# Kernel tuning notes

Measured on AMD Instinct MI355X. Metric: run time of the kernel, lower is better.

The kernel has to match this reference:

```python
import jax, jax.numpy as jnp
import numpy as np

D_MODEL = 1024
NUM_HEADS = 16
D_K = D_MODEL // NUM_HEADS
D_FF = 4096
EPS = 1e-5


def setup_inputs() -> dict:
    key = jax.random.key(0)
    ks = jax.random.split(key, 16)
    B, S = 2, 2048
    s_attn = 1.0 / np.sqrt(D_MODEL)
    s_ff1 = 1.0 / np.sqrt(D_MODEL)
    s_ff2 = 1.0 / np.sqrt(D_FF)
    return {
        "x": jax.random.normal(ks[0], (B, S, D_MODEL), jnp.float32),
        "Wq": jax.random.normal(ks[1], (D_MODEL, D_MODEL), jnp.float32) * s_attn,
        "bq": jnp.zeros((D_MODEL,), jnp.float32),
        "Wk": jax.random.normal(ks[2], (D_MODEL, D_MODEL), jnp.float32) * s_attn,
        "bk": jnp.zeros((D_MODEL,), jnp.float32),
        "Wv": jax.random.normal(ks[3], (D_MODEL, D_MODEL), jnp.float32) * s_attn,
        "bv": jnp.zeros((D_MODEL,), jnp.float32),
        "Wo": jax.random.normal(ks[4], (D_MODEL, D_MODEL), jnp.float32) * s_attn,
        "bo": jnp.zeros((D_MODEL,), jnp.float32),
        "W1": jax.random.normal(ks[5], (D_MODEL, D_FF), jnp.float32) * s_ff1,
        "b1": jnp.zeros((D_FF,), jnp.float32),
        "W2": jax.random.normal(ks[6], (D_FF, D_MODEL), jnp.float32) * s_ff2,
        "b2": jnp.zeros((D_MODEL,), jnp.float32),
        "g1": jnp.ones((D_MODEL,), jnp.float32),
        "be1": jnp.zeros((D_MODEL,), jnp.float32),
        "g2": jnp.ones((D_MODEL,), jnp.float32),
        "be2": jnp.zeros((D_MODEL,), jnp.float32),
    }


def _layernorm(x, g, b):
    m = jnp.mean(x, axis=-1, keepdims=True)
    v = jnp.mean(jnp.square(x - m), axis=-1, keepdims=True)
    return (x - m) * jax.lax.rsqrt(v + EPS) * g + b


def _split_heads(x, B, S):
    # (B, S, D) -> (B, H, S, d_k)
    return x.reshape(B, S, NUM_HEADS, D_K).transpose(0, 2, 1, 3)


def reference(x, Wq, bq, Wk, bk, Wv, bv, Wo, bo, W1, b1, W2, b2, g1, be1, g2, be2):
    B, S, _ = x.shape
    Q = _split_heads(x @ Wq + bq, B, S)
    K = _split_heads(x @ Wk + bk, B, S)
    V = _split_heads(x @ Wv + bv, B, S)
    scores = jnp.einsum("bhqd,bhkd->bhqk", Q, K) / np.sqrt(D_K).astype(np.float32)
    attn = jax.nn.softmax(scores, axis=-1)  # dropout is identity (p=0 / eval)
    ctx = jnp.einsum("bhqk,bhkd->bhqd", attn, V)
    ctx = ctx.transpose(0, 2, 1, 3).reshape(B, S, D_MODEL)
    attn_out = ctx @ Wo + bo
    h = _layernorm(x + attn_out, g1, be1)
    ff = jax.nn.relu(h @ W1 + b1) @ W2 + b2
    out = _layernorm(h + ff, g2, be2)
    return out, attn
```

## Files before the change

kernel.cpp:

```cpp
#include <hip/hip_runtime.h>
#include <cstddef>
#include <cstdint>

#define D_MODEL 1024
#define NUM_HEADS 16
#define DK 64
#define D_FF 4096
#define SEQ 2048
#define BATCH 2
#define EPS 1e-5f

typedef unsigned short u16;
typedef __attribute__((ext_vector_type(8))) short bf16x8;
typedef __attribute__((ext_vector_type(8))) unsigned short us8;
typedef __attribute__((ext_vector_type(4))) unsigned short us4;
typedef __attribute__((ext_vector_type(4))) float f32x4;

#define SBAR() asm volatile("s_barrier" ::: "memory")

__device__ __forceinline__ u16 f2b(float f) {
    unsigned u = __float_as_uint(f);
    u += 0x7fffu + ((u >> 16) & 1u);
    return (u16)(u >> 16);
}
__device__ __forceinline__ float b2f(u16 v) {
    return __uint_as_float((unsigned)v << 16);
}

__device__ __forceinline__ void gload16(const void* g, void* l) {
    __builtin_amdgcn_global_load_lds(
        (const __attribute__((address_space(1))) void*)g,
        (__attribute__((address_space(3))) void*)l, 16, 0, 0);
}

__device__ __forceinline__ void stage_half(
    const u16* __restrict__ g, int ld, long kbase, int h,
    u16* dst, int tid, int wid)
{
#pragma unroll
    for (int r = 0; r < 2; ++r) {
        const int ci  = r * 512 + tid;
        const int row = ci >> 2;
        const int wd  = ci & 3;
        const int f   = (row + (row >> 2)) & 3;
        const long src = (long)row * ld + kbase + (long)(h * 4 + (wd ^ f)) * 8;
        gload16(g + src, dst + (r * 512 + wid * 64) * 8);
    }
}

__device__ __forceinline__ bf16x8 frag64(const u16* base, int ks, int row, int g) {
    const int f = (row + (row >> 2)) & 3;
    return *(const bf16x8*)&base[ks * 8192 + row * 32 + ((g ^ f) * 8)];
}

template<int KTOT, bool RELU>
__global__ __launch_bounds__(512, 2) void gemm256(
    const u16* __restrict__ Abf, const u16* __restrict__ BT,
    const float* __restrict__ bias0, u16* __restrict__ C0,
    int ldc, int nx)
{
    constexpr int NT = KTOT / 64;
    __shared__ u16 lds[2][32768];

    const int tid = threadIdx.x;
    const int wid = tid >> 6, l = tid & 63;
    const int r16 = l & 15, g = l >> 4;
    const int wr = wid >> 2, wc = wid & 3;

    const int nwg = gridDim.x;
    const int q = nwg >> 3, rr = nwg & 7;
    const int xcd = blockIdx.x & 7, idx = blockIdx.x >> 3;
    const int wg = (xcd < rr ? xcd * (q + 1) : rr * (q + 1) + (xcd - rr) * q) + idx;
    const long bm = (long)(wg / nx) * 256;
    const long bn = (long)(wg % nx) * 256;

    const u16* Ag = Abf + bm * KTOT;
    const u16* Bg = BT + bn * KTOT;

    f32x4 acc[8][4];
#pragma unroll
    for (int i = 0; i < 8; ++i)
#pragma unroll
        for (int n = 0; n < 4; ++n)
            acc[i][n] = (f32x4){0.f, 0.f, 0.f, 0.f};

    stage_half(Ag, KTOT, 0, 0, &lds[0][0],     tid, wid);
    stage_half(Ag, KTOT, 0, 1, &lds[0][8192],  tid, wid);
    stage_half(Bg, KTOT, 0, 0, &lds[0][16384], tid, wid);
    stage_half(Bg, KTOT, 0, 1, &lds[0][24576], tid, wid);
    if (NT > 1) {
        stage_half(Ag, KTOT, 64, 0, &lds[1][0],     tid, wid);
        stage_half(Bg, KTOT, 64, 0, &lds[1][16384], tid, wid);
    }
    asm volatile("s_waitcnt vmcnt(4)" ::: "memory");
    SBAR();

    for (int t = 0; t < NT; ++t) {
        u16* cur = &lds[t & 1][0];
        u16* nxt = &lds[(t + 1) & 1][0];
        const long k1 = (long)(t + 1) * 64;
        const long k2 = (long)(t + 2) * 64;
        const bool s1 = (t + 1 < NT), s2 = (t + 2 < NT);

        bf16x8 a0[4], b0[4];
#pragma unroll
        for (int i = 0; i < 4; ++i) {
            a0[i] = frag64(cur,         0, wr * 128 + i * 16 + r16, g);
            b0[i] = frag64(cur + 16384, 0, wc * 64  + i * 16 + r16, g);
        }
        if (s1) stage_half(Ag, KTOT, k1, 1, nxt + 8192, tid, wid);
        SBAR();
        __builtin_amdgcn_s_setprio(1);
#pragma unroll
        for (int i = 0; i < 4; ++i)
#pragma unroll
            for (int n = 0; n < 4; ++n)
                acc[i][n] = __builtin_amdgcn_mfma_f32_16x16x32_bf16(
                    a0[i], b0[n], acc[i][n], 0, 0, 0);
        __builtin_amdgcn_s_setprio(0);
        SBAR();

        bf16x8 a1[4];
#pragma unroll
        for (int i = 0; i < 4; ++i)
            a1[i] = frag64(cur, 0, wr * 128 + (i + 4) * 16 + r16, g);
        if (s1) stage_half(Bg, KTOT, k1, 1, nxt + 24576, tid, wid);
        SBAR();
        __builtin_amdgcn_s_setprio(1);
#pragma unroll
        for (int i = 0; i < 4; ++i)
#pragma unroll
            for (int n = 0; n < 4; ++n)
                acc[i + 4][n] = __builtin_amdgcn_mfma_f32_16x16x32_bf16(
                    a1[i], b0[n], acc[i + 4][n], 0, 0, 0);
        __builtin_amdgcn_s_setprio(0);
        SBAR();

        bf16x8 a2[4], b1[4];
#pragma unroll
        for (int i = 0; i < 4; ++i) {
            a2[i] = frag64(cur,         1, wr * 128 + i * 16 + r16, g);
            b1[i] = frag64(cur + 16384, 1, wc * 64  + i * 16 + r16, g);
        }
        if (s2) stage_half(Ag, KTOT, k2, 0, cur, tid, wid);
        SBAR();
        __builtin_amdgcn_s_setprio(1);
#pragma unroll
        for (int i = 0; i < 4; ++i)
#pragma unroll
            for (int n = 0; n < 4; ++n)
                acc[i][n] = __builtin_amdgcn_mfma_f32_16x16x32_bf16(
                    a2[i], b1[n], acc[i][n], 0, 0, 0);
        __builtin_amdgcn_s_setprio(0);
        SBAR();

        bf16x8 a3[4];
#pragma unroll
        for (int i = 0; i < 4; ++i)
            a3[i] = frag64(cur, 1, wr * 128 + (i + 4) * 16 + r16, g);
        if (s2) stage_half(Bg, KTOT, k2, 0, cur + 16384, tid, wid);
        SBAR();
        __builtin_amdgcn_s_setprio(1);
#pragma unroll
        for (int i = 0; i < 4; ++i)
#pragma unroll
            for (int n = 0; n < 4; ++n)
                acc[i + 4][n] = __builtin_amdgcn_mfma_f32_16x16x32_bf16(
                    a3[i], b1[n], acc[i + 4][n], 0, 0, 0);
        __builtin_amdgcn_s_setprio(0);
        if (s2)      asm volatile("s_waitcnt vmcnt(4)" ::: "memory");
        else if (s1) asm volatile("s_waitcnt vmcnt(0)" ::: "memory");
        SBAR();
    }

    const long crow0 = bm + wr * 128 + g * 4;
    const long ccol0 = bn + wc * 64 + r16;
#pragma unroll
    for (int n = 0; n < 4; ++n) {
        const long col = ccol0 + n * 16;
        const float bv = bias0[col];
#pragma unroll
        for (int i = 0; i < 8; ++i)
#pragma unroll
            for (int j = 0; j < 4; ++j) {
                const long row = crow0 + i * 16 + j;
                float v = acc[i][n][j] + bv;
                if (RELU) v = fmaxf(v, 0.f);
                C0[row * (long)ldc + col] = f2b(v);
            }
    }
}

template<bool RELU, int NSPLIT>
__global__ __launch_bounds__(256) void gemm_mfma(
    const u16* __restrict__ Abf, const u16* __restrict__ BT,
    const float* __restrict__ bias0, const float* __restrict__ bias1,
    const float* __restrict__ bias2,
    u16* __restrict__ C0, u16* __restrict__ C1, u16* __restrict__ C2,
    int lda, int ldb, int ldc, int K, int nx)
{
    constexpr int BM = 128, BN = 128;
    constexpr int MI = 4, NI = 4;
    constexpr int RA = 2, RB = 2;
    constexpr int TILE = (BM + BN) * 32;

    __shared__ u16 sm[2][TILE];

    const int tid = threadIdx.x;
    const int w = tid >> 6, l = tid & 63;
    const int r16 = l & 15, g = l >> 4;
    const int wr = w >> 1, wc = w & 1;

    const int nwg = gridDim.x;
    const int q = nwg >> 3, rr = nwg & 7;
    const int xcd = blockIdx.x & 7, idx = blockIdx.x >> 3;
    const int wg = (xcd < rr ? xcd * (q + 1) : rr * (q + 1) + (xcd - rr) * q) + idx;
    const long bm = (long)(wg / nx) * BM;
    const long bn = (long)(wg % nx) * BN;

    f32x4 acc[MI][NI];
#pragma unroll
    for (int mi = 0; mi < MI; ++mi)
#pragma unroll
        for (int ni = 0; ni < NI; ++ni)
            acc[mi][ni] = (f32x4){0.f, 0.f, 0.f, 0.f};

    long aOff[RA], bOff[RB];
#pragma unroll
    for (int r = 0; r < RA; ++r) {
        int c = r * 256 + tid;
        aOff[r] = (long)(bm + (c >> 2)) * lda + (c & 3) * 8;
    }
#pragma unroll
    for (int r = 0; r < RB; ++r) {
        int c = r * 256 + tid;
        bOff[r] = (long)(bn + (c >> 2)) * ldb + (c & 3) * 8;
    }

#pragma unroll
    for (int r = 0; r < RA; ++r)
        gload16(Abf + aOff[r], &sm[0][0] + (r * 256 + w * 64) * 8);
#pragma unroll
    for (int r = 0; r < RB; ++r)
        gload16(BT + bOff[r], &sm[0][BM * 32] + (r * 256 + w * 64) * 8);
    __syncthreads();

    int cur = 0;
    for (int k0 = 0; k0 < K; k0 += 32) {
        if (k0 + 32 < K) {
            const int nxt = cur ^ 1;
#pragma unroll
            for (int r = 0; r < RA; ++r)
                gload16(Abf + aOff[r] + k0 + 32, &sm[nxt][0] + (r * 256 + w * 64) * 8);
#pragma unroll
            for (int r = 0; r < RB; ++r)
                gload16(BT + bOff[r] + k0 + 32, &sm[nxt][BM * 32] + (r * 256 + w * 64) * 8);
        }

        const u16* smA = &sm[cur][0];
        const u16* smB = &sm[cur][BM * 32];
        bf16x8 af[MI], bfr[NI];
#pragma unroll
        for (int mi = 0; mi < MI; ++mi)
            af[mi] = *(const bf16x8*)&smA[(wr * 64 + mi * 16 + r16) * 32 + g * 8];
#pragma unroll
        for (int ni = 0; ni < NI; ++ni)
            bfr[ni] = *(const bf16x8*)&smB[(wc * 64 + ni * 16 + r16) * 32 + g * 8];
#pragma unroll
        for (int mi = 0; mi < MI; ++mi)
#pragma unroll
            for (int ni = 0; ni < NI; ++ni)
                acc[mi][ni] = __builtin_amdgcn_mfma_f32_16x16x32_bf16(
                    af[mi], bfr[ni], acc[mi][ni], 0, 0, 0);

        __syncthreads();
        cur ^= 1;
    }

    u16* Cb = C0; const float* bp = bias0; long coff = 0;
    if (NSPLIT == 3) {
        const int grp = (int)(bn >> 10);
        if (grp == 1)      { Cb = C1; bp = bias1; }
        else if (grp == 2) { Cb = C2; bp = bias2; }
        coff = (long)grp << 10;
    }
    const long crow0 = bm + wr * 64 + g * 4;
    const long ccol0 = bn + wc * 64 + r16 - coff;
#pragma unroll
    for (int ni = 0; ni < NI; ++ni) {
        const long col = ccol0 + ni * 16;
        const float bv = bp[col];
#pragma unroll
        for (int mi = 0; mi < MI; ++mi) {
#pragma unroll
            for (int j = 0; j < 4; ++j) {
                const long row = crow0 + mi * 16 + j;
                float v = acc[mi][ni][j] + bv;
                if (RELU) v = fmaxf(v, 0.f);
                Cb[row * (long)ldc + col] = f2b(v);
            }
        }
    }
}

template<bool RELU>
__global__ __launch_bounds__(256) void gemm_n64(
    const u16* __restrict__ Abf, const u16* __restrict__ BT,
    const float* __restrict__ bias, u16* __restrict__ C,
    int lda, int ldb, int ldc, int K, int nx)
{
    constexpr int BM = 128, BN = 64;
    constexpr int MI = 2, NI = 4;
    constexpr int RA = 2, RB = 1;
    constexpr int TILE = (BM + BN) * 32;

    __shared__ u16 sm[2][TILE];

    const int tid = threadIdx.x;
    const int w = tid >> 6, l = tid & 63;
    const int r16 = l & 15, g = l >> 4;

    const int nwg = gridDim.x;
    const int q = nwg >> 3, rr = nwg & 7;
    const int xcd = blockIdx.x & 7, idx = blockIdx.x >> 3;
    const int wg = (xcd < rr ? xcd * (q + 1) : rr * (q + 1) + (xcd - rr) * q) + idx;
    const long bm = (long)(wg / nx) * BM;
    const long bn = (long)(wg % nx) * BN;

    f32x4 acc[MI][NI];
#pragma unroll
    for (int mi = 0; mi < MI; ++mi)
#pragma unroll
        for (int ni = 0; ni < NI; ++ni)
            acc[mi][ni] = (f32x4){0.f, 0.f, 0.f, 0.f};

    long aOff[RA], bOff[RB];
#pragma unroll
    for (int r = 0; r < RA; ++r) {
        int c = r * 256 + tid;
        aOff[r] = (long)(bm + (c >> 2)) * lda + (c & 3) * 8;
    }
#pragma unroll
    for (int r = 0; r < RB; ++r) {
        int c = r * 256 + tid;
        bOff[r] = (long)(bn + (c >> 2)) * ldb + (c & 3) * 8;
    }

#pragma unroll
    for (int r = 0; r < RA; ++r)
        gload16(Abf + aOff[r], &sm[0][0] + (r * 256 + w * 64) * 8);
#pragma unroll
    for (int r = 0; r < RB; ++r)
        gload16(BT + bOff[r], &sm[0][BM * 32] + (r * 256 + w * 64) * 8);
    __syncthreads();

    int cur = 0;
    for (int k0 = 0; k0 < K; k0 += 32) {
        if (k0 + 32 < K) {
            const int nxt = cur ^ 1;
#pragma unroll
            for (int r = 0; r < RA; ++r)
                gload16(Abf + aOff[r] + k0 + 32, &sm[nxt][0] + (r * 256 + w * 64) * 8);
#pragma unroll
            for (int r = 0; r < RB; ++r)
                gload16(BT + bOff[r] + k0 + 32, &sm[nxt][BM * 32] + (r * 256 + w * 64) * 8);
        }

        const u16* smA = &sm[cur][0];
        const u16* smB = &sm[cur][BM * 32];
        bf16x8 af[MI], bfr[NI];
#pragma unroll
        for (int mi = 0; mi < MI; ++mi)
            af[mi] = *(const bf16x8*)&smA[(w * 32 + mi * 16 + r16) * 32 + g * 8];
#pragma unroll
        for (int ni = 0; ni < NI; ++ni)
            bfr[ni] = *(const bf16x8*)&smB[(ni * 16 + r16) * 32 + g * 8];
#pragma unroll
        for (int mi = 0; mi < MI; ++mi)
#pragma unroll
            for (int ni = 0; ni < NI; ++ni)
                acc[mi][ni] = __builtin_amdgcn_mfma_f32_16x16x32_bf16(
                    af[mi], bfr[ni], acc[mi][ni], 0, 0, 0);

        __syncthreads();
        cur ^= 1;
    }

    const long crow0 = bm + w * 32 + g * 4;
    const long ccol0 = bn + r16;
#pragma unroll
    for (int ni = 0; ni < NI; ++ni) {
        const long col = ccol0 + ni * 16;
        const float bv = bias[col];
#pragma unroll
        for (int mi = 0; mi < MI; ++mi) {
#pragma unroll
            for (int j = 0; j < 4; ++j) {
                const long row = crow0 + mi * 16 + j;
                float v = acc[mi][ni][j] + bv;
                if (RELU) v = fmaxf(v, 0.f);
                C[row * (long)ldc + col] = f2b(v);
            }
        }
    }
}

#define QBLK 128
#define KBLK 64
#define NTT (SEQ / KBLK)
#define C2E 0.18033688f

__global__ __launch_bounds__(256) void flash_attn(
    const u16* __restrict__ Qg, const u16* __restrict__ Kg,
    const u16* __restrict__ Vt, float* __restrict__ attn,
    u16* __restrict__ ctx)
{
    __shared__ u16 smem[16384];
    __shared__ u16 Ps[4][2048];

    u16* const Qs  = smem;
    u16* const kb0 = smem + 8192;
    u16* const kb1 = smem;

    const int tid = threadIdx.x;
    const int w = tid >> 6, l = tid & 63;
    const int r16 = l & 15, g = l >> 4;

    const int wg = (blockIdx.x & 7) * (gridDim.x >> 3) + (blockIdx.x >> 3);
    const int qb = wg & 15, z = wg >> 4;
    const int b = z >> 4, h = z & 15;
    const long q0 = (long)qb * QBLK;

    const long kBase = ((long)b * SEQ) * D_MODEL + h * DK;
    const long vBase = (long)z * DK * SEQ;

#pragma unroll
    for (int r = 0; r < 4; ++r) {
        int c = r * 256 + tid;
        int row = c >> 3, bl = c & 7;
        long src = ((long)b * SEQ + q0 + row) * D_MODEL + h * DK
                 + ((bl ^ (row & 7)) * 8);
        gload16(Qg + src, Qs + (r * 256 + w * 64) * 8);
    }
#pragma unroll
    for (int r = 0; r < 2; ++r) {
        int c = r * 256 + tid;
        int row = c >> 3, bl = c & 7;
        gload16(Kg + kBase + (long)row * D_MODEL + ((bl ^ (row & 7)) * 8),
                kb0 + (r * 256 + w * 64) * 8);
    }
    __syncthreads();

    bf16x8 qf[2][2];
#pragma unroll
    for (int qi = 0; qi < 2; ++qi)
#pragma unroll
        for (int ks = 0; ks < 2; ++ks)
            qf[qi][ks] = *(const bf16x8*)
                &Qs[(w * 32 + qi * 16 + r16) * 64 + (((ks * 4 + g) ^ (r16 & 7)) * 8)];
    __syncthreads();

    float lrun[2] = {0.f, 0.f};

    for (int t = 0; t < NTT; ++t) {
        if (t + 1 < NTT) {
            u16* kdst = ((t + 1) & 1) ? kb1 : kb0;
            const long kro = (long)(t + 1) * KBLK;
#pragma unroll
            for (int r = 0; r < 2; ++r) {
                int c = r * 256 + tid;
                int row = c >> 3, bl = c & 7;
                gload16(Kg + kBase + (kro + row) * D_MODEL + ((bl ^ (row & 7)) * 8),
                        kdst + (r * 256 + w * 64) * 8);
            }
        }
        const u16* kcur = (t & 1) ? kb1 : kb0;

        f32x4 sT[4][2];
#pragma unroll
        for (int ki = 0; ki < 4; ++ki)
#pragma unroll
            for (int qi = 0; qi < 2; ++qi) sT[ki][qi] = (f32x4){0.f, 0.f, 0.f, 0.f};

        __builtin_amdgcn_s_setprio(1);
#pragma unroll
        for (int ks = 0; ks < 2; ++ks) {
            bf16x8 kf[4];
#pragma unroll
            for (int ki = 0; ki < 4; ++ki)
                kf[ki] = *(const bf16x8*)
                    &kcur[(ki * 16 + r16) * 64 + (((ks * 4 + g) ^ (r16 & 7)) * 8)];
#pragma unroll
            for (int ki = 0; ki < 4; ++ki)
#pragma unroll
                for (int qi = 0; qi < 2; ++qi)
                    sT[ki][qi] = __builtin_amdgcn_mfma_f32_16x16x32_bf16(
                        kf[ki], qf[qi][ks], sT[ki][qi], 0, 0, 0);
        }
        __builtin_amdgcn_s_setprio(0);

#pragma unroll
        for (int qi = 0; qi < 2; ++qi) {
            float ls = 0.f;
#pragma unroll
            for (int ki = 0; ki < 4; ++ki)
#pragma unroll
                for (int j = 0; j < 4; ++j)
                    ls += exp2f(sT[ki][qi][j] * C2E);
            ls += __shfl_xor(ls, 16);
            ls += __shfl_xor(ls, 32);
            lrun[qi] += ls;
        }
        __syncthreads();
    }

    const float il[2] = {1.0f / lrun[0], 1.0f / lrun[1]};

    u16* const p2b0 = smem + 8192;
    u16* const p2b1 = smem;
#pragma unroll
    for (int r = 0; r < 2; ++r) {
        int c = r * 256 + tid;
        int row = c >> 3, bl = c & 7;
        gload16(Kg + kBase + (long)row * D_MODEL + ((bl ^ (row & 7)) * 8),
                p2b0 + (r * 256 + w * 64) * 8);
        gload16(Vt + vBase + (long)row * SEQ + ((bl ^ (row & 7)) * 8),
                p2b0 + 4096 + (r * 256 + w * 64) * 8);
    }
    __syncthreads();

    f32x4 acc2[2][4];
#pragma unroll
    for (int mi = 0; mi < 2; ++mi)
#pragma unroll
        for (int ni = 0; ni < 4; ++ni) acc2[mi][ni] = (f32x4){0.f, 0.f, 0.f, 0.f};

    const long arow0 = ((long)z * SEQ + q0 + w * 32) * (long)SEQ;

    for (int t = 0; t < NTT; ++t) {
        const int k0 = t * KBLK;
        if (t + 1 < NTT) {
            u16* dst = ((t + 1) & 1) ? p2b1 : p2b0;
            const long kro = (long)(t + 1) * KBLK;
#pragma unroll
            for (int r = 0; r < 2; ++r) {
                int c = r * 256 + tid;
                int row = c >> 3, bl = c & 7;
                gload16(Kg + kBase + (kro + row) * D_MODEL + ((bl ^ (row & 7)) * 8),
                        dst + (r * 256 + w * 64) * 8);
                gload16(Vt + vBase + (long)row * SEQ + kro + ((bl ^ (row & 7)) * 8),
                        dst + 4096 + (r * 256 + w * 64) * 8);
            }
        }
        const u16* kcur = (t & 1) ? p2b1 : p2b0;
        const u16* vcur = kcur + 4096;

        f32x4 sT[4][2];
#pragma unroll
        for (int ki = 0; ki < 4; ++ki)
#pragma unroll
            for (int qi = 0; qi < 2; ++qi) sT[ki][qi] = (f32x4){0.f, 0.f, 0.f, 0.f};

        __builtin_amdgcn_s_setprio(1);
#pragma unroll
        for (int ks = 0; ks < 2; ++ks) {
            bf16x8 kf[4];
#pragma unroll
            for (int ki = 0; ki < 4; ++ki)
                kf[ki] = *(const bf16x8*)
                    &kcur[(ki * 16 + r16) * 64 + (((ks * 4 + g) ^ (r16 & 7)) * 8)];
#pragma unroll
            for (int ki = 0; ki < 4; ++ki)
#pragma unroll
                for (int qi = 0; qi < 2; ++qi)
                    sT[ki][qi] = __builtin_amdgcn_mfma_f32_16x16x32_bf16(
                        kf[ki], qf[qi][ks], sT[ki][qi], 0, 0, 0);
        }
        __builtin_amdgcn_s_setprio(0);

#pragma unroll
        for (int qi = 0; qi < 2; ++qi) {
            const long ar = arow0 + (long)(qi * 16 + r16) * SEQ + k0 + g * 4;
            const int prow = (qi * 16 + r16) * 64;
#pragma unroll
            for (int ki = 0; ki < 4; ++ki) {
                f32x4 p;
                p[0] = exp2f(sT[ki][qi][0] * C2E) * il[qi];
                p[1] = exp2f(sT[ki][qi][1] * C2E) * il[qi];
                p[2] = exp2f(sT[ki][qi][2] * C2E) * il[qi];
                p[3] = exp2f(sT[ki][qi][3] * C2E) * il[qi];
                __builtin_nontemporal_store(p, (f32x4*)&attn[ar + ki * 16]);
                us4 pb;
                pb[0] = f2b(p[0]); pb[1] = f2b(p[1]);
                pb[2] = f2b(p[2]); pb[3] = f2b(p[3]);
                const int kblk = 2 * ki + (g >> 1);
                *(us4*)&Ps[w][prow + ((kblk ^ (r16 & 7)) << 3) + ((g & 1) << 2)] = pb;
            }
        }

        __builtin_amdgcn_s_setprio(1);
#pragma unroll
        for (int ks = 0; ks < 2; ++ks) {
            bf16x8 pf[2], vf[4];
#pragma unroll
            for (int mi = 0; mi < 2; ++mi)
                pf[mi] = *(const bf16x8*)
                    &Ps[w][(mi * 16 + r16) * 64 + (((ks * 4 + g) ^ (r16 & 7)) << 3)];
#pragma unroll
            for (int ni = 0; ni < 4; ++ni)
                vf[ni] = *(const bf16x8*)
                    &vcur[(ni * 16 + r16) * 64 + (((ks * 4 + g) ^ (r16 & 7)) * 8)];
#pragma unroll
            for (int mi = 0; mi < 2; ++mi)
#pragma unroll
                for (int ni = 0; ni < 4; ++ni)
                    acc2[mi][ni] = __builtin_amdgcn_mfma_f32_16x16x32_bf16(
                        pf[mi], vf[ni], acc2[mi][ni], 0, 0, 0);
        }
        __builtin_amdgcn_s_setprio(0);
        __syncthreads();
    }

#pragma unroll
    for (int mi = 0; mi < 2; ++mi)
#pragma unroll
        for (int j = 0; j < 4; ++j) {
            const long grow = (long)b * SEQ + q0 + w * 32 + mi * 16 + g * 4 + j;
#pragma unroll
            for (int ni = 0; ni < 4; ++ni)
                ctx[grow * D_MODEL + h * DK + ni * 16 + r16] = f2b(acc2[mi][ni][j]);
        }
}

__device__ __forceinline__ void tr32(
    const float* __restrict__ W, u16* __restrict__ Wt, int R, int C,
    int bx, int by, int tx, int ty, float (*t)[33])
{
    const long c = (long)bx * 32 + tx;
    const long r0 = (long)by * 32;
#pragma unroll
    for (int j = 0; j < 32; j += 8)
        t[ty + j][tx] = W[(r0 + ty + j) * C + c];
    __syncthreads();
    const long r = r0 + tx;
#pragma unroll
    for (int j = 0; j < 32; j += 8)
        Wt[((long)bx * 32 + ty + j) * R + r] = f2b(t[tx][ty + j]);
}

__global__ __launch_bounds__(256) void preproc(
    const float* __restrict__ x, u16* __restrict__ x_bf,
    const float* __restrict__ Wq, const float* __restrict__ Wk,
    const float* __restrict__ Wv, const float* __restrict__ Wo,
    u16* __restrict__ Wqkvo_t,
    const float* __restrict__ W1, u16* __restrict__ W1t,
    const float* __restrict__ W2, u16* __restrict__ W2t)
{
    __shared__ float t[32][33];
    int bid = blockIdx.x;
    const int tx = threadIdx.x & 31, ty = threadIdx.x >> 5;

    if (bid < 2048) {
        long i = ((long)bid * 256 + threadIdx.x) * 8;
        float4 a = *(const float4*)(x + i);
        float4 b = *(const float4*)(x + i + 4);
        us8 o;
        o[0] = f2b(a.x); o[1] = f2b(a.y); o[2] = f2b(a.z); o[3] = f2b(a.w);
        o[4] = f2b(b.x); o[5] = f2b(b.y); o[6] = f2b(b.z); o[7] = f2b(b.w);
        *(us8*)(x_bf + i) = o;
        return;
    }
    bid -= 2048;
    if (bid < 4096) {
        const int z = bid >> 10, rem = bid & 1023;
        const float* W = (z == 0) ? Wq : (z == 1) ? Wk : (z == 2) ? Wv : Wo;
        tr32(W, Wqkvo_t + (size_t)z * D_MODEL * D_MODEL, D_MODEL, D_MODEL,
             rem & 31, rem >> 5, tx, ty, t);
        return;
    }
    bid -= 4096;
    if (bid < 4096) {
        tr32(W1, W1t, D_MODEL, D_FF, bid & 127, bid >> 7, tx, ty, t);
        return;
    }
    bid -= 4096;
    {
        tr32(W2, W2t, D_FF, D_MODEL, bid & 31, bid >> 5, tx, ty, t);
    }
}

__global__ __launch_bounds__(256) void transpose_v(
    const u16* __restrict__ V, u16* __restrict__ Vt)
{
    __shared__ u16 t[32][33];
    const int z = blockIdx.z, b = z >> 4, h = z & 15;
    const int tx = threadIdx.x & 31, ty = threadIdx.x >> 5;
    const long k0 = (long)blockIdx.x * 32;
    const long d0 = (long)blockIdx.y * 32;
#pragma unroll
    for (int j = 0; j < 32; j += 8)
        t[ty + j][tx] = V[((long)b * SEQ + k0 + ty + j) * D_MODEL + h * DK + d0 + tx];
    __syncthreads();
#pragma unroll
    for (int j = 0; j < 32; j += 8)
        Vt[((long)z * DK + d0 + ty + j) * SEQ + k0 + tx] = t[tx][ty + j];
}

template<int OM>
__global__ __launch_bounds__(256) void add_ln_kernel(
    const u16* __restrict__ a, const u16* __restrict__ b,
    const float* __restrict__ g, const float* __restrict__ be,
    void* __restrict__ outp)
{
    const int l = threadIdx.x & 63, w = threadIdx.x >> 6;
    const long row = (long)blockIdx.x * 4 + w;
    const long base = row * D_MODEL;

    float xv[16];
#pragma unroll
    for (int c = 0; c < 2; ++c) {
        const long off = c * 512 + l * 8;
        us8 av = *(const us8*)(a + base + off);
        us8 bv = *(const us8*)(b + base + off);
#pragma unroll
        for (int i = 0; i < 8; ++i)
            xv[c * 8 + i] = b2f(av[i]) + b2f(bv[i]);
    }

    float s = 0.f;
#pragma unroll
    for (int i = 0; i < 16; ++i) s += xv[i];
#pragma unroll
    for (int off = 1; off < 64; off <<= 1) s += __shfl_xor(s, off);
    const float mean = s * (1.0f / D_MODEL);

    float ss = 0.f;
#pragma unroll
    for (int i = 0; i < 16; ++i) {
        xv[i] -= mean;
        ss += xv[i] * xv[i];
    }
#pragma unroll
    for (int off = 1; off < 64; off <<= 1) ss += __shfl_xor(ss, off);
    const float rs = rsqrtf(ss * (1.0f / D_MODEL) + EPS);

#pragma unroll
    for (int c = 0; c < 2; ++c) {
        const long off = c * 512 + l * 8;
        float4 g0 = *(const float4*)(g + off);
        float4 g1 = *(const float4*)(g + off + 4);
        float4 b0 = *(const float4*)(be + off);
        float4 b1 = *(const float4*)(be + off + 4);
        float o[8];
        o[0] = xv[c*8+0] * rs * g0.x + b0.x;
        o[1] = xv[c*8+1] * rs * g0.y + b0.y;
        o[2] = xv[c*8+2] * rs * g0.z + b0.z;
        o[3] = xv[c*8+3] * rs * g0.w + b0.w;
        o[4] = xv[c*8+4] * rs * g1.x + b1.x;
        o[5] = xv[c*8+5] * rs * g1.y + b1.y;
        o[6] = xv[c*8+6] * rs * g1.z + b1.z;
        o[7] = xv[c*8+7] * rs * g1.w + b1.w;
        if (OM == 0) {
            float4 v0 = {o[0], o[1], o[2], o[3]};
            float4 v1 = {o[4], o[5], o[6], o[7]};
            *(float4*)((float*)outp + base + off) = v0;
            *(float4*)((float*)outp + base + off + 4) = v1;
        } else {
            us8 ob;
#pragma unroll
            for (int i = 0; i < 8; ++i) ob[i] = f2b(o[i]);
            *(us8*)((u16*)outp + base + off) = ob;
        }
    }
}

extern "C" void kernel_launch(void* const* d_in, const int* in_sizes, int n_in,
                              void* d_out, int out_size, void* d_ws, size_t ws_size,
                              hipStream_t stream)
{
    const float* x   = (const float*)d_in[0];
    const float* Wq  = (const float*)d_in[1];
    const float* bq  = (const float*)d_in[2];
    const float* Wk  = (const float*)d_in[3];
    const float* bk  = (const float*)d_in[4];
    const float* Wv  = (const float*)d_in[5];
    const float* bv  = (const float*)d_in[6];
    const float* Wo  = (const float*)d_in[7];
    const float* bo  = (const float*)d_in[8];
    const float* W1  = (const float*)d_in[9];
    const float* b1  = (const float*)d_in[10];
    const float* W2  = (const float*)d_in[11];
    const float* b2  = (const float*)d_in[12];
    const float* g1  = (const float*)d_in[13];
    const float* be1 = (const float*)d_in[14];
    const float* g2  = (const float*)d_in[15];
    const float* be2 = (const float*)d_in[16];

    float* out  = (float*)d_out;
    float* attn = out + (size_t)BATCH * SEQ * D_MODEL;

    char* ws = (char*)d_ws;
    const size_t MB = 1u << 20;
    u16* x_bf    = (u16*)(ws);
    u16* Q_bf    = (u16*)(ws + 8 * MB);
    u16* K_bf    = (u16*)(ws + 16 * MB);
    u16* Vt      = (u16*)(ws + 24 * MB);
    u16* V_bf    = (u16*)(ws + 32 * MB);
    u16* Wqkvo_t = (u16*)(ws + 40 * MB);
    u16* W1t     = (u16*)(ws + 48 * MB);
    u16* W2t     = (u16*)(ws + 56 * MB);
    u16* ff1_bf  = (u16*)(ws + 64 * MB);
    u16* ctx_bf  = (u16*)(ws + 96 * MB);
    u16* Wot     = Wqkvo_t + (size_t)3 * D_MODEL * D_MODEL;
    u16* h_bf    = K_bf;
    u16* ao_bf   = V_bf;
    u16* ff2_bf  = Vt;

    const int M = BATCH * SEQ;
    dim3 T(256);

    preproc<<<dim3(2048 + 3 * 4096), T, 0, stream>>>(
        x, x_bf, Wq, Wk, Wv, Wo, Wqkvo_t, W1, W1t, W2, W2t);

    gemm_mfma<false, 3><<<dim3((M / 128) * 24), T, 0, stream>>>(
        x_bf, Wqkvo_t, bq, bk, bv, Q_bf, K_bf, V_bf,
        D_MODEL, D_MODEL, D_MODEL, D_MODEL, 24);

    transpose_v<<<dim3(SEQ / 32, DK / 32, BATCH * NUM_HEADS), T, 0, stream>>>(V_bf, Vt);

    flash_attn<<<dim3((SEQ / QBLK) * BATCH * NUM_HEADS), T, 0, stream>>>(
        Q_bf, K_bf, Vt, attn, ctx_bf);

    gemm_n64<false><<<dim3((M / 128) * 16), T, 0, stream>>>(
        ctx_bf, Wot, bo, ao_bf, D_MODEL, D_MODEL, D_MODEL, D_MODEL, 16);

    add_ln_kernel<1><<<dim3(M / 4), T, 0, stream>>>(x_bf, ao_bf, g1, be1, h_bf);

    gemm256<D_MODEL, true><<<dim3((M / 256) * (D_FF / 256)), dim3(512), 0, stream>>>(
        h_bf, W1t, b1, ff1_bf, D_FF, D_FF / 256);

    gemm_n64<false><<<dim3((M / 128) * 16), T, 0, stream>>>(
        ff1_bf, W2t, b2, ff2_bf, D_FF, D_FF, D_MODEL, D_FF, 16);

    add_ln_kernel<0><<<dim3(M / 4), T, 0, stream>>>(h_bf, ff2_bf, g2, be2, out);
}
```

Measured before the change: 409.7 us.

## Triple-buffer GEMM LDS tiles and relax vmcnt waits for deeper prefetch

Both GEMM kernels move from double to triple buffering of shared-memory tiles. Each loads two k-steps ahead and waits with partial vmcnt counts instead of a full __syncthreads drain, so global loads for later tiles stay in flight across the barrier. The attention loop likewise replaces its end-of-iteration __syncthreads with a partial vmcnt wait plus barrier, and skips it on the last iteration. This costs more LDS per block, which may lower occupancy, and correctness depends on the hand-tuned vmcnt counts matching the number of outstanding loads.

```diff
diff --git a/kernel.cpp b/kernel.cpp
--- a/kernel.cpp
+++ b/kernel.cpp
@@ -204,7 +204,7 @@
     constexpr int RA = 2, RB = 2;
     constexpr int TILE = (BM + BN) * 32;
 
-    __shared__ u16 sm[2][TILE];
+    __shared__ u16 sm[3][TILE];
 
     const int tid = threadIdx.x;
     const int w = tid >> 6, l = tid & 63;
@@ -243,18 +243,27 @@
 #pragma unroll
     for (int r = 0; r < RB; ++r)
         gload16(BT + bOff[r], &sm[0][BM * 32] + (r * 256 + w * 64) * 8);
-    __syncthreads();
+    if (K > 32) {
+#pragma unroll
+        for (int r = 0; r < RA; ++r)
+            gload16(Abf + aOff[r] + 32, &sm[1][0] + (r * 256 + w * 64) * 8);
+#pragma unroll
+        for (int r = 0; r < RB; ++r)
+            gload16(BT + bOff[r] + 32, &sm[1][BM * 32] + (r * 256 + w * 64) * 8);
+    }
+    asm volatile("s_waitcnt vmcnt(4)" ::: "memory");
+    SBAR();
 
     int cur = 0;
     for (int k0 = 0; k0 < K; k0 += 32) {
-        if (k0 + 32 < K) {
-            const int nxt = cur ^ 1;
+        const int nx2 = (cur >= 1) ? cur - 1 : cur + 2;
+        if (k0 + 64 < K) {
 #pragma unroll
             for (int r = 0; r < RA; ++r)
-                gload16(Abf + aOff[r] + k0 + 32, &sm[nxt][0] + (r * 256 + w * 64) * 8);
+                gload16(Abf + aOff[r] + k0 + 64, &sm[nx2][0] + (r * 256 + w * 64) * 8);
 #pragma unroll
             for (int r = 0; r < RB; ++r)
-                gload16(BT + bOff[r] + k0 + 32, &sm[nxt][BM * 32] + (r * 256 + w * 64) * 8);
+                gload16(BT + bOff[r] + k0 + 64, &sm[nx2][BM * 32] + (r * 256 + w * 64) * 8);
         }
 
         const u16* smA = &sm[cur][0];
@@ -273,8 +282,10 @@
                 acc[mi][ni] = __builtin_amdgcn_mfma_f32_16x16x32_bf16(
                     af[mi], bfr[ni], acc[mi][ni], 0, 0, 0);
 
-        __syncthreads();
-        cur ^= 1;
+        if (k0 + 64 < K)      asm volatile("s_waitcnt vmcnt(4)" ::: "memory");
+        else if (k0 + 32 < K) asm volatile("s_waitcnt vmcnt(0)" ::: "memory");
+        SBAR();
+        cur = (cur == 2) ? 0 : cur + 1;
     }
 
     u16* Cb = C0; const float* bp = bias0; long coff = 0;
@@ -314,7 +325,7 @@
     constexpr int RA = 2, RB = 1;
     constexpr int TILE = (BM + BN) * 32;
 
-    __shared__ u16 sm[2][TILE];
+    __shared__ u16 sm[3][TILE];
 
     const int tid = threadIdx.x;
     const int w = tid >> 6, l = tid & 63;
@@ -352,18 +363,27 @@
 #pragma unroll
     for (int r = 0; r < RB; ++r)
         gload16(BT + bOff[r], &sm[0][BM * 32] + (r * 256 + w * 64) * 8);
-    __syncthreads();
+    if (K > 32) {
+#pragma unroll
+        for (int r = 0; r < RA; ++r)
+            gload16(Abf + aOff[r] + 32, &sm[1][0] + (r * 256 + w * 64) * 8);
+#pragma unroll
+        for (int r = 0; r < RB; ++r)
+            gload16(BT + bOff[r] + 32, &sm[1][BM * 32] + (r * 256 + w * 64) * 8);
+    }
+    asm volatile("s_waitcnt vmcnt(3)" ::: "memory");
+    SBAR();
 
     int cur = 0;
     for (int k0 = 0; k0 < K; k0 += 32) {
-        if (k0 + 32 < K) {
-            const int nxt = cur ^ 1;
+        const int nx2 = (cur >= 1) ? cur - 1 : cur + 2;
+        if (k0 + 64 < K) {
 #pragma unroll
             for (int r = 0; r < RA; ++r)
-                gload16(Abf + aOff[r] + k0 + 32, &sm[nxt][0] + (r * 256 + w * 64) * 8);
+                gload16(Abf + aOff[r] + k0 + 64, &sm[nx2][0] + (r * 256 + w * 64) * 8);
 #pragma unroll
             for (int r = 0; r < RB; ++r)
-                gload16(BT + bOff[r] + k0 + 32, &sm[nxt][BM * 32] + (r * 256 + w * 64) * 8);
+                gload16(BT + bOff[r] + k0 + 64, &sm[nx2][BM * 32] + (r * 256 + w * 64) * 8);
         }
 
         const u16* smA = &sm[cur][0];
@@ -382,8 +402,10 @@
                 acc[mi][ni] = __builtin_amdgcn_mfma_f32_16x16x32_bf16(
                     af[mi], bfr[ni], acc[mi][ni], 0, 0, 0);
 
-        __syncthreads();
-        cur ^= 1;
+        if (k0 + 64 < K)      asm volatile("s_waitcnt vmcnt(3)" ::: "memory");
+        else if (k0 + 32 < K) asm volatile("s_waitcnt vmcnt(0)" ::: "memory");
+        SBAR();
+        cur = (cur == 2) ? 0 : cur + 1;
     }
 
     const long crow0 = bm + w * 32 + g * 4;
@@ -618,7 +640,11 @@
                         pf[mi], vf[ni], acc2[mi][ni], 0, 0, 0);
         }
         __builtin_amdgcn_s_setprio(0);
-        __syncthreads();
+
+        if (t + 1 < NTT) {
+            asm volatile("s_waitcnt vmcnt(8)" ::: "memory");
+            SBAR();
+        }
     }
 
 #pragma unroll
```

New measurement: 399.0 us. 2.6% less time.
